# Kernel optimization log

Measured on AMD Instinct MI355X. Metric: run time of the kernel, lower is better.

## Reference

```python
import jax, jax.numpy as jnp
import numpy as np

NUM_CAPSULE = 32
DIM_CAPSULE = 16
ROUTINGS = 3
EPS = 1e-7        # K.epsilon()
L2_EPS = 1e-12    # tf.nn.l2_normalize epsilon


def squash(x, axis=-1):
    s = jnp.sum(jnp.square(x), axis=axis, keepdims=True) + EPS
    scale = jnp.sqrt(s) / (0.5 + s)
    return scale * x


def setup_inputs() -> dict:
    key = jax.random.key(0)
    k1, k2 = jax.random.split(key)
    B, N_in, D_in = 64, 2048, 64
    u_vecs = jax.random.normal(k1, (B, N_in, D_in), dtype=jnp.float32)
    # glorot-ish scale for the 1x1 conv kernel (1, D_in, num_capsule*dim_capsule)
    kernel = jax.random.normal(k2, (1, D_in, NUM_CAPSULE * DIM_CAPSULE), dtype=jnp.float32)
    kernel = kernel * np.sqrt(2.0 / (D_in + NUM_CAPSULE * DIM_CAPSULE)).astype(np.float32)
    return {"u_vecs": u_vecs, "kernel": kernel}


def reference(u_vecs, kernel):
    B, N_in, D_in = u_vecs.shape
    # K.conv1d with kernel_size=1 == matmul along the feature dim
    u_hat = jnp.einsum('bnd,dm->bnm', u_vecs, kernel[0])
    # (B, N_in, num_cap, dim_cap) -> (B, num_cap, N_in, dim_cap)
    u_hat = u_hat.reshape(B, N_in, NUM_CAPSULE, DIM_CAPSULE).transpose(0, 2, 1, 3)

    b = jnp.zeros((B, NUM_CAPSULE, N_in), dtype=u_hat.dtype)
    o = None
    for i in range(ROUTINGS):
        c = jax.nn.softmax(b, axis=1)                 # softmax over output capsules
        o = jnp.einsum('bin,binj->bij', c, u_hat)     # (B, num_cap, dim_cap)
        if i < ROUTINGS - 1:
            norm = jnp.sqrt(jnp.maximum(jnp.sum(jnp.square(o), axis=-1, keepdims=True), L2_EPS))
            o = o / norm                              # K.l2_normalize(o, -1)
            b = jnp.einsum('bij,binj->bin', o, u_hat)  # b = <v, u_hat> (non-accumulating)
    return squash(o)
```

## Files before the change

### kernel.cpp

```cpp
#include <hip/hip_runtime.h>
#include <hip/hip_bf16.h>


#define BB 64
#define NN 2048
#define DD 64
#define II 32
#define JJ 16
#define RR 256

__global__ __launch_bounds__(256) void ksum(const float* __restrict__ u,
                                            float* __restrict__ s) {
    int b = blockIdx.y;
    int cb = blockIdx.x;
    int d = threadIdx.x & 63;
    int g = threadIdx.x >> 6;
    const float* ub = u + (size_t)b * NN * DD + (size_t)(cb * 64) * DD;
    float acc = 0.f;
    #pragma unroll 4
    for (int r = g; r < 64; r += 4)
        acc += ub[(size_t)r * DD + d];
    __shared__ float red[4][64];
    red[g][d] = acc;
    __syncthreads();
    if (g == 0)
        atomicAdd(&s[b * DD + d], red[0][d] + red[1][d] + red[2][d] + red[3][d]);
}

template <int MODE>
__global__ __launch_bounds__(512) void ksmall(const float* __restrict__ src,
                                              const float* __restrict__ W,
                                              float* __restrict__ w_out,
                                              float* __restrict__ out) {
    int b = blockIdx.x;
    int tid = threadIdx.x;
    int i = tid >> 4;
    int j = tid & 15;
    const float* trow = (MODE == 0) ? (src + (size_t)b * DD)
                                    : (src + ((size_t)b * II + i) * DD);
    float o = 0.f;
    #pragma unroll 8
    for (int d = 0; d < DD; ++d)
        o += trow[d] * W[d * (II * JJ) + i * JJ + j];
    if (MODE == 0) o *= (1.0f / 32.0f);

    float ss = o * o;
    #pragma unroll
    for (int off = 8; off >= 1; off >>= 1)
        ss += __shfl_xor(ss, off, 16);

    if (MODE == 2) {
        float s2 = ss + 1e-7f;
        float scale = sqrtf(s2) / (0.5f + s2);
        out[((size_t)b * II + i) * JJ + j] = scale * o;
        return;
    }

    float norm = sqrtf(fmaxf(ss, 1e-12f));
    float ov = o / norm;
    __shared__ float osh[II][JJ];
    osh[i][j] = ov;
    __syncthreads();
    #pragma unroll
    for (int k = 0; k < 4; ++k) {
        int d = j + 16 * k;
        float acc = 0.f;
        #pragma unroll
        for (int jj = 0; jj < 16; ++jj)
            acc += W[d * (II * JJ) + i * JJ + jj] * osh[i][jj];
        w_out[((size_t)b * II + i) * DD + d] = acc;
    }
}

__global__ __launch_bounds__(256, 2) void kbig(const float* __restrict__ u,
                                               const float* __restrict__ w,
                                               float* __restrict__ t) {
    int b = blockIdx.y;
    int chunk = blockIdx.x;
    const float* ub = u + (size_t)b * NN * DD;
    const float* wb = w + (size_t)b * II * DD;

    __shared__ __align__(16) float wsh[II][68];
    __shared__ __align__(16) float csh[II][RR + 4];
    int tid = threadIdx.x;

    for (int idx = tid; idx < II * DD; idx += 256)
        wsh[idx >> 6][idx & 63] = wb[idx];
    __syncthreads();

    int h = tid & 1;
    int p = tid >> 1;
    int nbase = chunk * RR + 2 * p;
    const float* ra = ub + (size_t)nbase * DD;
    const float* rb = ra + DD;
    float bacc[2][16];
    #pragma unroll
    for (int il = 0; il < 16; ++il) { bacc[0][il] = 0.f; bacc[1][il] = 0.f; }

    #pragma unroll 4
    for (int d0 = 0; d0 < DD; d0 += 4) {
        float4 ua = *reinterpret_cast<const float4*>(ra + d0);
        float4 ub4 = *reinterpret_cast<const float4*>(rb + d0);
        #pragma unroll
        for (int il = 0; il < 16; ++il) {
            float4 w4 = *reinterpret_cast<const float4*>(&wsh[h * 16 + il][d0]);
            bacc[0][il] += ua.x * w4.x + ua.y * w4.y + ua.z * w4.z + ua.w * w4.w;
            bacc[1][il] += ub4.x * w4.x + ub4.y * w4.y + ub4.z * w4.z + ub4.w * w4.w;
        }
    }

    #pragma unroll
    for (int r = 0; r < 2; ++r) {
        float m = bacc[r][0];
        #pragma unroll
        for (int il = 1; il < 16; ++il) m = fmaxf(m, bacc[r][il]);
        m = fmaxf(m, __shfl_xor(m, 1));
        float sum = 0.f;
        #pragma unroll
        for (int il = 0; il < 16; ++il) { bacc[r][il] = __expf(bacc[r][il] - m); sum += bacc[r][il]; }
        sum += __shfl_xor(sum, 1);
        float inv = 1.f / sum;
        #pragma unroll
        for (int il = 0; il < 16; ++il)
            csh[h * 16 + il][2 * p + r] = bacc[r][il] * inv;
    }
    __syncthreads();

    int d = tid & 63;
    int wv = tid >> 6;
    const float* up = ub + (size_t)(chunk * RR + wv * 64) * DD + d;
    float tacc[32];
    #pragma unroll
    for (int i = 0; i < II; ++i) tacc[i] = 0.f;

    for (int n0 = 0; n0 < 64; n0 += 4) {
        float u0 = up[(size_t)(n0 + 0) * DD];
        float u1 = up[(size_t)(n0 + 1) * DD];
        float u2 = up[(size_t)(n0 + 2) * DD];
        float u3 = up[(size_t)(n0 + 3) * DD];
        int nn = wv * 64 + n0;
        #pragma unroll
        for (int i = 0; i < II; ++i) {
            float4 c4 = *reinterpret_cast<const float4*>(&csh[i][nn]);
            tacc[i] += c4.x * u0 + c4.y * u1 + c4.z * u2 + c4.w * u3;
        }
    }
    float* tb = t + ((size_t)b * II) * DD + d;
    #pragma unroll
    for (int i = 0; i < II; ++i)
        atomicAdd(tb + (size_t)i * DD, tacc[i]);
}

extern "C" void kernel_launch(void* const* d_in, const int* in_sizes, int n_in,
                              void* d_out, int out_size, void* d_ws, size_t ws_size,
                              hipStream_t stream) {
    const float* u = (const float*)d_in[0];
    const float* W = (const float*)d_in[1];
    float* out = (float*)d_out;
    float* ws = (float*)d_ws;

    float* s  = ws;
    float* t1 = ws + 4096;
    float* t2 = ws + 4096 + 131072;
    float* wv = ws + 4096 + 2 * 131072;

    hipMemsetAsync(ws, 0, (4096 + 2 * 131072) * sizeof(float), stream);

    ksum<<<dim3(32, BB), 256, 0, stream>>>(u, s);
    ksmall<0><<<BB, 512, 0, stream>>>(s, W, wv, nullptr);
    kbig<<<dim3(NN / RR, BB), 256, 0, stream>>>(u, wv, t1);
    ksmall<1><<<BB, 512, 0, stream>>>(t1, W, wv, nullptr);
    kbig<<<dim3(NN / RR, BB), 256, 0, stream>>>(u, wv, t2);
    ksmall<2><<<BB, 512, 0, stream>>>(t2, W, nullptr, out);
}
```

Baseline: 118.6 us.

## Use bf16 MFMA for routing logits and split-bf16 MFMA for weighted sum

Rewrites the main routing kernel to compute the 32-capsule logits with 32x32x16 bf16 MFMA instructions in place of scalar FMA loops. It also computes the softmax-weighted reduction over u with MFMA, splitting coefficients and inputs into hi/lo bf16 parts (three products) to keep near-fp32 accuracy. Partial results are reduced in LDS with shared atomics before the global atomics. Chunk size drops to 128 rows, which doubles the grid. The goal is to turn the compute-bound inner loops into matrix-core work. The trade-off is that the logits use plain bf16, which adds rounding error before the softmax, and the u loads are strided scalar reads.

```diff
diff --git a/kernel.cpp b/kernel.cpp
--- a/kernel.cpp
+++ b/kernel.cpp
@@ -7,7 +7,19 @@
 #define DD 64
 #define II 32
 #define JJ 16
-#define RR 256
+#define CHROWS 128
+
+typedef __attribute__((ext_vector_type(8)))  short bf16x8;
+typedef __attribute__((ext_vector_type(16))) float f32x16;
+
+__device__ inline short f2bf(float f) {
+    __hip_bfloat16 h = __float2bfloat16(f);
+    return *reinterpret_cast<short*>(&h);
+}
+__device__ inline float bf2f(short s) {
+    __hip_bfloat16 h = *reinterpret_cast<__hip_bfloat16*>(&s);
+    return __bfloat162float(h);
+}
 
 __global__ __launch_bounds__(256) void ksum(const float* __restrict__ u,
                                             float* __restrict__ s) {
@@ -72,83 +84,117 @@
     }
 }
 
-__global__ __launch_bounds__(256, 2) void kbig(const float* __restrict__ u,
-                                               const float* __restrict__ w,
-                                               float* __restrict__ t) {
+__global__ __launch_bounds__(256) void kbig(const float* __restrict__ u,
+                                            const float* __restrict__ w,
+                                            float* __restrict__ t) {
     int b = blockIdx.y;
     int chunk = blockIdx.x;
-    const float* ub = u + (size_t)b * NN * DD;
-    const float* wb = w + (size_t)b * II * DD;
-
-    __shared__ __align__(16) float wsh[II][68];
-    __shared__ __align__(16) float csh[II][RR + 4];
     int tid = threadIdx.x;
-
-    for (int idx = tid; idx < II * DD; idx += 256)
-        wsh[idx >> 6][idx & 63] = wb[idx];
-    __syncthreads();
-
-    int h = tid & 1;
-    int p = tid >> 1;
-    int nbase = chunk * RR + 2 * p;
-    const float* ra = ub + (size_t)nbase * DD;
-    const float* rb = ra + DD;
-    float bacc[2][16];
-    #pragma unroll
-    for (int il = 0; il < 16; ++il) { bacc[0][il] = 0.f; bacc[1][il] = 0.f; }
-
-    #pragma unroll 4
-    for (int d0 = 0; d0 < DD; d0 += 4) {
-        float4 ua = *reinterpret_cast<const float4*>(ra + d0);
-        float4 ub4 = *reinterpret_cast<const float4*>(rb + d0);
+    int wv = tid >> 6;
+    int l  = tid & 63;
+    int h  = l >> 5;
+    int ln = l & 31;
+
+    __shared__ float clds[CHROWS][II + 1];
+    __shared__ float tlds[II][DD + 1];
+
+    float* tldsf = &tlds[0][0];
+    for (int k = tid; k < II * (DD + 1); k += 256) tldsf[k] = 0.f;
+
+    const float* wbase = w + (size_t)b * II * DD;
+    int nrow = chunk * CHROWS + wv * 32 + ln;
+    const float* urow = u + ((size_t)b * NN + nrow) * DD;
+    const float* wrow = wbase + (size_t)ln * DD;
+
+    f32x16 S;
+    #pragma unroll
+    for (int r = 0; r < 16; ++r) S[r] = 0.f;
+
+    #pragma unroll
+    for (int kt = 0; kt < 4; ++kt) {
+        int dofs = kt * 16 + h * 8;
+        float4 a0 = *reinterpret_cast<const float4*>(wrow + dofs);
+        float4 a1 = *reinterpret_cast<const float4*>(wrow + dofs + 4);
+        float4 b0 = *reinterpret_cast<const float4*>(urow + dofs);
+        float4 b1 = *reinterpret_cast<const float4*>(urow + dofs + 4);
+        bf16x8 A, Bv;
+        A[0]=f2bf(a0.x); A[1]=f2bf(a0.y); A[2]=f2bf(a0.z); A[3]=f2bf(a0.w);
+        A[4]=f2bf(a1.x); A[5]=f2bf(a1.y); A[6]=f2bf(a1.z); A[7]=f2bf(a1.w);
+        Bv[0]=f2bf(b0.x); Bv[1]=f2bf(b0.y); Bv[2]=f2bf(b0.z); Bv[3]=f2bf(b0.w);
+        Bv[4]=f2bf(b1.x); Bv[5]=f2bf(b1.y); Bv[6]=f2bf(b1.z); Bv[7]=f2bf(b1.w);
+        S = __builtin_amdgcn_mfma_f32_32x32x16_bf16(A, Bv, S, 0, 0, 0);
+    }
+
+    float m = S[0];
+    #pragma unroll
+    for (int r = 1; r < 16; ++r) m = fmaxf(m, S[r]);
+    m = fmaxf(m, __shfl_xor(m, 32));
+    float sum = 0.f;
+    float e[16];
+    #pragma unroll
+    for (int r = 0; r < 16; ++r) { e[r] = __expf(S[r] - m); sum += e[r]; }
+    sum += __shfl_xor(sum, 32);
+    float inv = 1.f / sum;
+    #pragma unroll
+    for (int r = 0; r < 16; ++r) {
+        int irow = (r & 3) + 8 * (r >> 2) + 4 * h;
+        clds[wv * 32 + ln][irow] = e[r] * inv;
+    }
+    __syncthreads();
+
+    f32x16 G0, G1;
+    #pragma unroll
+    for (int r = 0; r < 16; ++r) { G0[r] = 0.f; G1[r] = 0.f; }
+
+    bf16x8 Ah[2], Al[2];
+    #pragma unroll
+    for (int t2 = 0; t2 < 2; ++t2) {
+        int nb = wv * 32 + t2 * 16 + h * 8;
         #pragma unroll
-        for (int il = 0; il < 16; ++il) {
-            float4 w4 = *reinterpret_cast<const float4*>(&wsh[h * 16 + il][d0]);
-            bacc[0][il] += ua.x * w4.x + ua.y * w4.y + ua.z * w4.z + ua.w * w4.w;
-            bacc[1][il] += ub4.x * w4.x + ub4.y * w4.y + ub4.z * w4.z + ub4.w * w4.w;
+        for (int jj = 0; jj < 8; ++jj) {
+            float cv = clds[nb + jj][ln];
+            short hi = f2bf(cv);
+            Ah[t2][jj] = hi;
+            Al[t2][jj] = f2bf(cv - bf2f(hi));
         }
     }
 
     #pragma unroll
-    for (int r = 0; r < 2; ++r) {
-        float m = bacc[r][0];
+    for (int t2 = 0; t2 < 2; ++t2) {
+        int ng = chunk * CHROWS + wv * 32 + t2 * 16 + h * 8;
         #pragma unroll
-        for (int il = 1; il < 16; ++il) m = fmaxf(m, bacc[r][il]);
-        m = fmaxf(m, __shfl_xor(m, 1));
-        float sum = 0.f;
-        #pragma unroll
-        for (int il = 0; il < 16; ++il) { bacc[r][il] = __expf(bacc[r][il] - m); sum += bacc[r][il]; }
-        sum += __shfl_xor(sum, 1);
-        float inv = 1.f / sum;
-        #pragma unroll
-        for (int il = 0; il < 16; ++il)
-            csh[h * 16 + il][2 * p + r] = bacc[r][il] * inv;
-    }
-    __syncthreads();
-
-    int d = tid & 63;
-    int wv = tid >> 6;
-    const float* up = ub + (size_t)(chunk * RR + wv * 64) * DD + d;
-    float tacc[32];
-    #pragma unroll
-    for (int i = 0; i < II; ++i) tacc[i] = 0.f;
-
-    for (int n0 = 0; n0 < 64; n0 += 4) {
-        float u0 = up[(size_t)(n0 + 0) * DD];
-        float u1 = up[(size_t)(n0 + 1) * DD];
-        float u2 = up[(size_t)(n0 + 2) * DD];
-        float u3 = up[(size_t)(n0 + 3) * DD];
-        int nn = wv * 64 + n0;
-        #pragma unroll
-        for (int i = 0; i < II; ++i) {
-            float4 c4 = *reinterpret_cast<const float4*>(&csh[i][nn]);
-            tacc[i] += c4.x * u0 + c4.y * u1 + c4.z * u2 + c4.w * u3;
+        for (int Nt = 0; Nt < 2; ++Nt) {
+            const float* ucol = u + ((size_t)b * NN + ng) * DD + Nt * 32 + ln;
+            bf16x8 Bh, Bl;
+            #pragma unroll
+            for (int jj = 0; jj < 8; ++jj) {
+                float uv = ucol[(size_t)jj * DD];
+                short hi = f2bf(uv);
+                Bh[jj] = hi;
+                Bl[jj] = f2bf(uv - bf2f(hi));
+            }
+            if (Nt == 0) {
+                G0 = __builtin_amdgcn_mfma_f32_32x32x16_bf16(Ah[t2], Bh, G0, 0, 0, 0);
+                G0 = __builtin_amdgcn_mfma_f32_32x32x16_bf16(Al[t2], Bh, G0, 0, 0, 0);
+                G0 = __builtin_amdgcn_mfma_f32_32x32x16_bf16(Ah[t2], Bl, G0, 0, 0, 0);
+            } else {
+                G1 = __builtin_amdgcn_mfma_f32_32x32x16_bf16(Ah[t2], Bh, G1, 0, 0, 0);
+                G1 = __builtin_amdgcn_mfma_f32_32x32x16_bf16(Al[t2], Bh, G1, 0, 0, 0);
+                G1 = __builtin_amdgcn_mfma_f32_32x32x16_bf16(Ah[t2], Bl, G1, 0, 0, 0);
+            }
         }
     }
-    float* tb = t + ((size_t)b * II) * DD + d;
-    #pragma unroll
-    for (int i = 0; i < II; ++i)
-        atomicAdd(tb + (size_t)i * DD, tacc[i]);
+
+    #pragma unroll
+    for (int r = 0; r < 16; ++r) {
+        int irow = (r & 3) + 8 * (r >> 2) + 4 * h;
+        atomicAdd(&tlds[irow][ln],      G0[r]);
+        atomicAdd(&tlds[irow][32 + ln], G1[r]);
+    }
+    __syncthreads();
+    for (int k = tid; k < II * DD; k += 256) {
+        atomicAdd(&t[(size_t)b * II * DD + k], tlds[k >> 6][k & 63]);
+    }
 }
 
 extern "C" void kernel_launch(void* const* d_in, const int* in_sizes, int n_in,
@@ -159,17 +205,17 @@
     float* out = (float*)d_out;
     float* ws = (float*)d_ws;
 
-    float* s  = ws;
-    float* t1 = ws + 4096;
-    float* t2 = ws + 4096 + 131072;
-    float* wv = ws + 4096 + 2 * 131072;
+    float* s    = ws;
+    float* t1   = ws + 4096;
+    float* t2   = ws + 4096 + 131072;
+    float* wtil = ws + 4096 + 2 * 131072;
 
     hipMemsetAsync(ws, 0, (4096 + 2 * 131072) * sizeof(float), stream);
 
     ksum<<<dim3(32, BB), 256, 0, stream>>>(u, s);
-    ksmall<0><<<BB, 512, 0, stream>>>(s, W, wv, nullptr);
-    kbig<<<dim3(NN / RR, BB), 256, 0, stream>>>(u, wv, t1);
-    ksmall<1><<<BB, 512, 0, stream>>>(t1, W, wv, nullptr);
-    kbig<<<dim3(NN / RR, BB), 256, 0, stream>>>(u, wv, t2);
+    ksmall<0><<<BB, 512, 0, stream>>>(s, W, wtil, nullptr);
+    kbig<<<dim3(NN / CHROWS, BB), 256, 0, stream>>>(u, wtil, t1);
+    ksmall<1><<<BB, 512, 0, stream>>>(t1, W, wtil, nullptr);
+    kbig<<<dim3(NN / CHROWS, BB), 256, 0, stream>>>(u, wtil, t2);
     ksmall<2><<<BB, 512, 0, stream>>>(t2, W, nullptr, out);
 }
```

Result: slower. 138.3 us (+16.7%).
